# Optimization experiments

Measured on AMD Instinct MI355X. Metric: run time of the kernel, lower is better.

The kernel has to match this reference:

```python
import jax, jax.numpy as jnp
import numpy as np

B, N, NC = 16, 102000, 35        # batch, raw YOLOv7@1280 predictions, num classes
IMG = 1280                        # input image size
CONF_THRESH = 0.25
IOU_THRESH = 0.45
PRE_TOPK = 1024                   # candidates kept before IoU suppression (yolov7 max_nms analogue)
MAX_DET = 300                     # padded detections per image (yolov7 max_det)


def setup_inputs() -> dict:
    key = jax.random.key(0)
    kxy, kwh, kobj, kcls = jax.random.split(key, 4)
    xy = jax.random.uniform(kxy, (B, N, 2), dtype=jnp.float32) * IMG        # box centers in pixels
    wh = jax.random.uniform(kwh, (B, N, 2), dtype=jnp.float32) * 96.0 + 4.0  # box sizes
    obj = jax.random.uniform(kobj, (B, N, 1), dtype=jnp.float32)            # objectness
    cls = jax.random.uniform(kcls, (B, N, NC), dtype=jnp.float32)           # class scores
    pred = jnp.concatenate([xy, wh, obj, cls], axis=-1)  # [B, N, 5+NC]
    return {"pred": pred}


def _xywh2xyxy(xywh):
    xy, wh = xywh[..., :2], xywh[..., 2:4]
    return jnp.concatenate([xy - wh * 0.5, xy + wh * 0.5], axis=-1)


def _iou_matrix(b):
    # b: [K, 4] xyxy -> [K, K] pairwise IoU
    area = jnp.clip(b[:, 2] - b[:, 0], 0.0) * jnp.clip(b[:, 3] - b[:, 1], 0.0)
    lt = jnp.maximum(b[:, None, :2], b[None, :, :2])
    rb = jnp.minimum(b[:, None, 2:], b[None, :, 2:])
    wh = jnp.clip(rb - lt, 0.0)
    inter = wh[..., 0] * wh[..., 1]
    return inter / (area[:, None] + area[None, :] - inter + 1e-7)


def _nms_single(boxes, scores, cls_id):
    # boxes: [N,4] xyxy, scores: [N] (0 where below conf thresh), cls_id: [N] float
    s, idx = jax.lax.top_k(scores, PRE_TOPK)
    b = boxes[idx]
    c = cls_id[idx]
    iou = _iou_matrix(b)              # [K, K]
    valid = s > 0.0
    ar = jnp.arange(PRE_TOPK)

    def body(suppressed, i):
        keep_i = valid[i] & ~suppressed[i]
        suppressed = suppressed | (keep_i & (iou[i] > IOU_THRESH) & (ar > i))
        return suppressed, keep_i

    _, keep = jax.lax.scan(body, jnp.zeros(PRE_TOPK, bool), ar)
    final = jnp.where(keep, s, 0.0)
    fs, fidx = jax.lax.top_k(final, MAX_DET)
    # [MAX_DET, 6] = x1, y1, x2, y2, conf, cls (conf==0 rows are padding)
    return jnp.concatenate([b[fidx], fs[:, None], c[fidx][:, None]], axis=-1)


def reference(pred):
    # yolov7 non_max_suppression, class-agnostic, best-class per box
    boxes = _xywh2xyxy(pred[..., :4])                    # [B, N, 4]
    obj = pred[..., 4]                                   # [B, N]
    cls_scores = pred[..., 5:] * obj[..., None]          # obj_conf * cls_conf
    conf = jnp.max(cls_scores, axis=-1)                  # [B, N]
    cls_id = jnp.argmax(cls_scores, axis=-1).astype(pred.dtype)
    cand = (obj > CONF_THRESH) & (conf > CONF_THRESH)    # candidate filter
    scores = jnp.where(cand, conf, 0.0)
    return jax.vmap(_nms_single)(boxes, scores, cls_id)  # [B, MAX_DET, 6]
```

## Files before the change

### kernel.cpp

```cpp
#include <hip/hip_runtime.h>
#include <stdint.h>

#define BB 16
#define NN 102000
#define NCLS 35
#define RSTRIDE 40
#define PRE 1024
#define CAP 2048
#define MAXDET 300
#define NBUCK 4096
#define CONF_T 0.25f
#define IOU_T 0.45f
#define BUCK_BASE 0x3E800000u
#define SROWS 256
#define HI_BUCK 3584u
#define GL_CAP 16384
#define GCNT_STRIDE 64

#define SCORES_OFF ((size_t)0)
#define SCORES_BYTES ((size_t)BB * NN * 4)
#define GHIST_OFF (SCORES_OFF + SCORES_BYTES)
#define GHIST_BYTES ((size_t)BB * NBUCK * 4)
#define GCNT_OFF (GHIST_OFF + GHIST_BYTES)
#define GCNT_BYTES ((size_t)BB * GCNT_STRIDE * 4)
#define BOXES_OFF (GCNT_OFF + GCNT_BYTES)
#define BOXES_BYTES ((size_t)BB * PRE * 16)
#define SVAL_OFF (BOXES_OFF + BOXES_BYTES)
#define SVAL_BYTES ((size_t)BB * PRE * 4)
#define CLS_OFF (SVAL_OFF + SVAL_BYTES)
#define CLS_BYTES ((size_t)BB * PRE * 4)
#define MASK_OFF (CLS_OFF + CLS_BYTES)
#define MASK_BYTES ((size_t)BB * PRE * 16 * 8)
#define GLIST_OFF (MASK_OFF + MASK_BYTES)
#define GLIST_BYTES ((size_t)BB * GL_CAP * 8)

__device__ __forceinline__ int KS(int i) { return i + (i >> 4); }
#define CAPP (CAP + (CAP >> 4))

__global__ __launch_bounds__(256) void k_score(const float* __restrict__ pred,
                                               float* __restrict__ scores,
                                               unsigned int* __restrict__ ghist,
                                               unsigned int* __restrict__ gcnt,
                                               unsigned long long* __restrict__ glist) {
    __shared__ float4 lds4[SROWS * 9];
    __shared__ unsigned int sWaveCnt[4];
    __shared__ unsigned int sBase;
    int b = blockIdx.y, tid = threadIdx.x;
    int rowBase = blockIdx.x * SROWS;
    int nrows = NN - rowBase; if (nrows > SROWS) nrows = SROWS;
    const float4* gp = (const float4*)(pred + ((size_t)b * NN + rowBase) * RSTRIDE);
    int nf4 = nrows * 9;
    for (int it = tid; it < nf4; it += 256) {
        int r = it / 9;
        int c = it - r * 9;
        lds4[r * 9 + c] = gp[r * 10 + 1 + c];
    }
    __syncthreads();
    float score = 0.0f;
    unsigned int bits = 0u, bk = 0u;
    if (tid < nrows) {
        const float4* row4 = &lds4[tid * 9];
        float4 v0 = row4[0];
        float obj = v0.x;
        if (obj > CONF_T) {
            float best = v0.y * obj;
            best = fmaxf(best, v0.z * obj);
            best = fmaxf(best, v0.w * obj);
#pragma unroll
            for (int c = 1; c < 9; ++c) {
                float4 v = row4[c];
                best = fmaxf(best, v.x * obj);
                best = fmaxf(best, v.y * obj);
                best = fmaxf(best, v.z * obj);
                best = fmaxf(best, v.w * obj);
            }
            if (best > CONF_T) score = best;
        }
        scores[(size_t)b * NN + rowBase + tid] = score;
        if (score > 0.0f) {
            bits = __float_as_uint(score);
            bk = (bits - BUCK_BASE) >> 12;
            if (bk > NBUCK - 1u) bk = NBUCK - 1u;
            atomicAdd(&ghist[b * NBUCK + bk], 1u);
        }
    }
    bool want = (score > 0.0f) && (bk >= HI_BUCK);
    unsigned long long m = __ballot(want);
    int lane = tid & 63, w = tid >> 6;
    if (lane == 0) sWaveCnt[w] = (unsigned int)__popcll(m);
    __syncthreads();
    if (tid == 0) {
        unsigned int tot = sWaveCnt[0] + sWaveCnt[1] + sWaveCnt[2] + sWaveCnt[3];
        sBase = tot ? atomicAdd(&gcnt[b * GCNT_STRIDE], tot) : 0u;
    }
    __syncthreads();
    if (want) {
        unsigned int pos = sBase;
        for (int k = 0; k < w; ++k) pos += sWaveCnt[k];
        pos += (unsigned int)__popcll(m & ((1ull << lane) - 1ull));
        if (pos < GL_CAP)
            glist[(size_t)b * GL_CAP + pos] =
                ((unsigned long long)bits << 32) |
                (unsigned int)(~(unsigned int)(rowBase + tid));
    }
}

__global__ __launch_bounds__(1024) void k_sort(const float* __restrict__ scores,
                                               const unsigned int* __restrict__ ghist,
                                               const unsigned int* __restrict__ gcnt,
                                               const unsigned long long* __restrict__ glist,
                                               const float* __restrict__ pred,
                                               float4* __restrict__ boxesWS,
                                               float* __restrict__ svalWS,
                                               float* __restrict__ clsWS) {
    __shared__ int sA[1024], sB[1024];
    __shared__ int cutSh;
    __shared__ unsigned long long keys[CAPP];
    __shared__ unsigned int nloc;
    int b = blockIdx.x, tid = threadIdx.x;

    const unsigned int* gh = ghist + b * NBUCK;
    int h0 = gh[4 * tid + 0], h1 = gh[4 * tid + 1];
    int h2 = gh[4 * tid + 2], h3 = gh[4 * tid + 3];
    if (tid == 0) { cutSh = 0; nloc = 0u; }
    sA[tid] = h0 + h1 + h2 + h3;
    for (int k = tid; k < CAP; k += 1024) keys[KS(k)] = 0ull;
    __syncthreads();
    int* src = sA;
    int* dst = sB;
    for (int off = 1; off < 1024; off <<= 1) {
        int x = src[tid];
        if (tid + off < 1024) x += src[tid + off];
        dst[tid] = x;
        __syncthreads();
        int* t_ = src; src = dst; dst = t_;
    }
    int nxt = (tid + 1 < 1024) ? src[tid + 1] : 0;
    int s3 = h3 + nxt;
    int s2 = h2 + s3;
    int s1 = h1 + s2;
    int s0 = h0 + s1;
    if (s0 >= PRE && s1 < PRE) cutSh = 4 * tid + 0;
    if (s1 >= PRE && s2 < PRE) cutSh = 4 * tid + 1;
    if (s2 >= PRE && s3 < PRE) cutSh = 4 * tid + 2;
    if (s3 >= PRE && nxt < PRE) cutSh = 4 * tid + 3;
    __syncthreads();
    unsigned int cut = (unsigned int)cutSh;
    unsigned int gn = gcnt[b * GCNT_STRIDE];

    if (cut >= HI_BUCK && gn <= (unsigned int)GL_CAP) {
        int n = (int)gn;
        const unsigned long long* gl = glist + (size_t)b * GL_CAP;
        for (int it = tid; it < n; it += 1024) {
            unsigned long long key = gl[it];
            unsigned int bits = (unsigned int)(key >> 32);
            unsigned int bk = (bits - BUCK_BASE) >> 12;
            if (bk > NBUCK - 1u) bk = NBUCK - 1u;
            if (bk >= cut) {
                unsigned int pos = atomicAdd(&nloc, 1u);
                if (pos < CAP) keys[KS((int)pos)] = key;
            }
        }
    } else {
        const float4* sb4 = (const float4*)(scores + (size_t)b * NN);
        for (int it = tid; it < NN / 4; it += 1024) {
            float4 s4 = sb4[it];
            float sv[4] = {s4.x, s4.y, s4.z, s4.w};
#pragma unroll
            for (int u = 0; u < 4; ++u) {
                float s = sv[u];
                if (s > 0.0f) {
                    unsigned int bits = __float_as_uint(s);
                    unsigned int bk = (bits - BUCK_BASE) >> 12;
                    if (bk > NBUCK - 1u) bk = NBUCK - 1u;
                    if (bk >= cut) {
                        unsigned int pos = atomicAdd(&nloc, 1u);
                        unsigned int idx = (unsigned int)(it * 4 + u);
                        if (pos < CAP)
                            keys[KS((int)pos)] = ((unsigned long long)bits << 32) |
                                                 (unsigned int)(~idx);
                    }
                }
            }
        }
    }
    __syncthreads();

    for (int k = 2; k <= CAP; k <<= 1) {
        for (int j = k >> 1; j > 0; j >>= 1) {
            int p = ((tid & ~(j - 1)) << 1) | (tid & (j - 1));
            int q = p | j;
            int pp = KS(p), qq = KS(q);
            unsigned long long a = keys[pp], c = keys[qq];
            bool desc = (p & k) == 0;
            bool sw = desc ? (a < c) : (a > c);
            if (sw) { keys[pp] = c; keys[qq] = a; }
            __syncthreads();
        }
    }

    unsigned long long key = keys[KS(tid)];
    unsigned int bits = (unsigned int)(key >> 32);
    unsigned int idx = ~(unsigned int)key;
    float sc = __uint_as_float(bits);
    if (bits == 0u || idx >= NN) { idx = 0; sc = 0.0f; }
    const float4* row = (const float4*)(pred + ((size_t)b * NN + idx) * RSTRIDE);
    float4 r0 = row[0];
    float4 r1 = row[1];
    float obj = r1.x;
    float best = r1.y * obj; int bj = 0;
    float p1 = r1.z * obj; if (p1 > best) { best = p1; bj = 1; }
    float p2 = r1.w * obj; if (p2 > best) { best = p2; bj = 2; }
#pragma unroll
    for (int kk = 2; kk <= 9; ++kk) {
        float4 r = row[kk];
        int base = (kk - 2) * 4 + 3;
        float q0 = r.x * obj; if (q0 > best) { best = q0; bj = base + 0; }
        float q1 = r.y * obj; if (q1 > best) { best = q1; bj = base + 1; }
        float q2 = r.z * obj; if (q2 > best) { best = q2; bj = base + 2; }
        float q3 = r.w * obj; if (q3 > best) { best = q3; bj = base + 3; }
    }
    float hx = r0.z * 0.5f;
    float hy = r0.w * 0.5f;
    boxesWS[b * PRE + tid] = make_float4(r0.x - hx, r0.y - hy, r0.x + hx, r0.y + hy);
    svalWS[b * PRE + tid] = sc;
    clsWS[b * PRE + tid] = (float)bj;
}

__global__ __launch_bounds__(256) void k_mask(const float4* __restrict__ boxesWS,
                                              const float* __restrict__ svalWS,
                                              unsigned long long* __restrict__ maskC) {
    __shared__ float bx1[PRE], by1[PRE], bx2[PRE], by2[PRE], bar[PRE], bsv[PRE];
    int b = blockIdx.y, tid = threadIdx.x;
    for (int i = tid; i < PRE; i += 256) {
        float4 bx = boxesWS[b * PRE + i];
        bx1[i] = bx.x; by1[i] = bx.y; bx2[i] = bx.z; by2[i] = bx.w;
        float aw = fmaxf(bx.z - bx.x, 0.0f);
        float ah = fmaxf(bx.w - bx.y, 0.0f);
        bar[i] = aw * ah;
        bsv[i] = svalWS[b * PRE + i];
    }
    __syncthreads();
    int j = blockIdx.x * 4 + (tid >> 6);
    int lane = tid & 63;
    float jx1 = bx1[j], jy1 = by1[j], jx2 = bx2[j], jy2 = by2[j], ja = bar[j];
    unsigned long long* out = maskC + ((size_t)b * PRE + j) * 16;
    for (int c = 0; c < 16; ++c) {
        unsigned long long word = 0ull;
        if (c * 64 < j) {
            int i = c * 64 + lane;
            bool bit = false;
            if (i < j && bsv[i] > 0.0f) {
                float ltx = fmaxf(bx1[i], jx1), lty = fmaxf(by1[i], jy1);
                float rbx = fminf(bx2[i], jx2), rby = fminf(by2[i], jy2);
                float wx = fmaxf(rbx - ltx, 0.0f);
                float wy = fmaxf(rby - lty, 0.0f);
                float inter = wx * wy;
                float denom = ((bar[i] + ja) - inter) + 1e-7f;
                bit = (inter / denom) > IOU_T;
            }
            word = __ballot(bit);
        }
        if (lane == 0) out[c] = word;
    }
}

__global__ __launch_bounds__(1024) void k_nms_out(const float4* __restrict__ boxesWS,
                                                  const float* __restrict__ svalWS,
                                                  const float* __restrict__ clsWS,
                                                  const unsigned long long* __restrict__ maskC,
                                                  float* __restrict__ out) {
    __shared__ unsigned long long supp[16];
    __shared__ int lastch;
    __shared__ int wtot[16], woff[17];
    int b = blockIdx.x, tid = threadIdx.x;
    int lane = tid & 63, w = tid >> 6;
    unsigned long long cm[16];
    const unsigned long long* mrow = maskC + ((size_t)b * PRE + tid) * 16;
#pragma unroll
    for (int k = 0; k < 16; ++k) cm[k] = mrow[k];
    float sv = svalWS[b * PRE + tid];
    if (tid < 16) supp[tid] = 0ull;
    if (tid == 0) lastch = -1;
    __syncthreads();
    for (int it = 0; it < PRE + 2; ++it) {
        bool nb = false;
#pragma unroll
        for (int k = 0; k < 16; ++k) nb |= ((cm[k] & ~supp[k]) != 0ull);
        unsigned long long word = __ballot(nb);
        __syncthreads();
        if (lane == 0) {
            if (word != supp[w]) lastch = it;
            supp[w] = word;
        }
        __syncthreads();
        if (lastch != it) break;
    }
    bool keep = (sv > 0.0f) && !((supp[w] >> lane) & 1ull);
    unsigned long long km = __ballot(keep);
    int lp = __popcll(km & ((lane == 0) ? 0ull : ((1ull << lane) - 1ull)));
    if (lane == 0) wtot[w] = __popcll(km);
    __syncthreads();
    if (tid == 0) {
        int acc = 0;
        for (int k = 0; k < 16; ++k) { woff[k] = acc; acc += wtot[k]; }
        woff[16] = acc;
    }
    __syncthreads();
    int K = woff[16];
    int keptExcl = woff[w] + lp;
    int slot = keep ? keptExcl : (K + (tid - keptExcl));
    if (slot < MAXDET) {
        float4 bx = boxesWS[b * PRE + tid];
        float cv = clsWS[b * PRE + tid];
        float* o = out + ((size_t)b * MAXDET + slot) * 6;
        o[0] = bx.x; o[1] = bx.y; o[2] = bx.z; o[3] = bx.w;
        o[4] = keep ? sv : 0.0f;
        o[5] = cv;
    }
}

extern "C" void kernel_launch(void* const* d_in, const int* in_sizes, int n_in,
                              void* d_out, int out_size, void* d_ws, size_t ws_size,
                              hipStream_t stream) {
    const float* pred = (const float*)d_in[0];
    float* out = (float*)d_out;
    char* ws = (char*)d_ws;
    float* scores = (float*)(ws + SCORES_OFF);
    unsigned int* ghist = (unsigned int*)(ws + GHIST_OFF);
    unsigned int* gcnt = (unsigned int*)(ws + GCNT_OFF);
    float4* boxesWS = (float4*)(ws + BOXES_OFF);
    float* svalWS = (float*)(ws + SVAL_OFF);
    float* clsWS = (float*)(ws + CLS_OFF);
    unsigned long long* maskC = (unsigned long long*)(ws + MASK_OFF);
    unsigned long long* glist = (unsigned long long*)(ws + GLIST_OFF);

    hipMemsetAsync(ws + GHIST_OFF, 0, GHIST_BYTES + GCNT_BYTES, stream);
    k_score<<<dim3((NN + SROWS - 1) / SROWS, BB), 256, 0, stream>>>(pred, scores, ghist,
                                                                   gcnt, glist);
    k_sort<<<BB, 1024, 0, stream>>>(scores, ghist, gcnt, glist, pred,
                                    boxesWS, svalWS, clsWS);
    k_mask<<<dim3(PRE / 4, BB), 256, 0, stream>>>(boxesWS, svalWS, maskC);
    k_nms_out<<<BB, 1024, 0, stream>>>(boxesWS, svalWS, clsWS, maskC, out);
}
```

Measured before the change: 426.7 us.

## Fuse sort, IoU mask and NMS output into one per-image kernel

Merges the sort/gather, IoU mask construction and greedy suppression/output kernels into a single kernel per image, keeping boxes, scores, classes and the suppression mask in registers and LDS instead of global workspace. Each thread now builds its own mask row serially over earlier candidates, replacing the wave-ballot mask kernel. This removes two launches and global round trips but concentrates the quadratic IoU work on only 16 blocks with triangular per-thread imbalance.

```diff
diff --git a/kernel.cpp b/kernel.cpp
--- a/kernel.cpp
+++ b/kernel.cpp
@@ -23,15 +23,7 @@
 #define GHIST_BYTES ((size_t)BB * NBUCK * 4)
 #define GCNT_OFF (GHIST_OFF + GHIST_BYTES)
 #define GCNT_BYTES ((size_t)BB * GCNT_STRIDE * 4)
-#define BOXES_OFF (GCNT_OFF + GCNT_BYTES)
-#define BOXES_BYTES ((size_t)BB * PRE * 16)
-#define SVAL_OFF (BOXES_OFF + BOXES_BYTES)
-#define SVAL_BYTES ((size_t)BB * PRE * 4)
-#define CLS_OFF (SVAL_OFF + SVAL_BYTES)
-#define CLS_BYTES ((size_t)BB * PRE * 4)
-#define MASK_OFF (CLS_OFF + CLS_BYTES)
-#define MASK_BYTES ((size_t)BB * PRE * 16 * 8)
-#define GLIST_OFF (MASK_OFF + MASK_BYTES)
+#define GLIST_OFF (GCNT_OFF + GCNT_BYTES)
 #define GLIST_BYTES ((size_t)BB * GL_CAP * 8)
 
 __device__ __forceinline__ int KS(int i) { return i + (i >> 4); }
@@ -105,19 +97,23 @@
     }
 }
 
-__global__ __launch_bounds__(1024) void k_sort(const float* __restrict__ scores,
-                                               const unsigned int* __restrict__ ghist,
-                                               const unsigned int* __restrict__ gcnt,
-                                               const unsigned long long* __restrict__ glist,
-                                               const float* __restrict__ pred,
-                                               float4* __restrict__ boxesWS,
-                                               float* __restrict__ svalWS,
-                                               float* __restrict__ clsWS) {
+__global__ __launch_bounds__(1024) void k_fused(const float* __restrict__ scores,
+                                                const unsigned int* __restrict__ ghist,
+                                                const unsigned int* __restrict__ gcnt,
+                                                const unsigned long long* __restrict__ glist,
+                                                const float* __restrict__ pred,
+                                                float* __restrict__ out) {
     __shared__ int sA[1024], sB[1024];
+    __shared__ unsigned long long keys[CAPP];
+    __shared__ float bx1[PRE], by1[PRE], bx2[PRE], by2[PRE], bar[PRE], bsv[PRE];
+    __shared__ float scls[PRE];
     __shared__ int cutSh;
-    __shared__ unsigned long long keys[CAPP];
     __shared__ unsigned int nloc;
+    __shared__ unsigned long long supp[16];
+    __shared__ int lastch;
+    __shared__ int wtot[16], woff[17];
     int b = blockIdx.x, tid = threadIdx.x;
+    int lane = tid & 63, w = tid >> 6;
 
     const unsigned int* gh = ghist + b * NBUCK;
     int h0 = gh[4 * tid + 0], h1 = gh[4 * tid + 1];
@@ -200,10 +196,10 @@
     }
 
     unsigned long long key = keys[KS(tid)];
-    unsigned int bits = (unsigned int)(key >> 32);
+    unsigned int kbits = (unsigned int)(key >> 32);
     unsigned int idx = ~(unsigned int)key;
-    float sc = __uint_as_float(bits);
-    if (bits == 0u || idx >= NN) { idx = 0; sc = 0.0f; }
+    float sc = __uint_as_float(kbits);
+    if (kbits == 0u || idx >= NN) { idx = 0; sc = 0.0f; }
     const float4* row = (const float4*)(pred + ((size_t)b * NN + idx) * RSTRIDE);
     float4 r0 = row[0];
     float4 r1 = row[1];
@@ -222,67 +218,40 @@
     }
     float hx = r0.z * 0.5f;
     float hy = r0.w * 0.5f;
-    boxesWS[b * PRE + tid] = make_float4(r0.x - hx, r0.y - hy, r0.x + hx, r0.y + hy);
-    svalWS[b * PRE + tid] = sc;
-    clsWS[b * PRE + tid] = (float)bj;
-}
-
-__global__ __launch_bounds__(256) void k_mask(const float4* __restrict__ boxesWS,
-                                              const float* __restrict__ svalWS,
-                                              unsigned long long* __restrict__ maskC) {
-    __shared__ float bx1[PRE], by1[PRE], bx2[PRE], by2[PRE], bar[PRE], bsv[PRE];
-    int b = blockIdx.y, tid = threadIdx.x;
-    for (int i = tid; i < PRE; i += 256) {
-        float4 bx = boxesWS[b * PRE + i];
-        bx1[i] = bx.x; by1[i] = bx.y; bx2[i] = bx.z; by2[i] = bx.w;
-        float aw = fmaxf(bx.z - bx.x, 0.0f);
-        float ah = fmaxf(bx.w - bx.y, 0.0f);
-        bar[i] = aw * ah;
-        bsv[i] = svalWS[b * PRE + i];
-    }
-    __syncthreads();
-    int j = blockIdx.x * 4 + (tid >> 6);
-    int lane = tid & 63;
-    float jx1 = bx1[j], jy1 = by1[j], jx2 = bx2[j], jy2 = by2[j], ja = bar[j];
-    unsigned long long* out = maskC + ((size_t)b * PRE + j) * 16;
+    float x1 = r0.x - hx, y1 = r0.y - hy, x2 = r0.x + hx, y2 = r0.y + hy;
+    bx1[tid] = x1; by1[tid] = y1; bx2[tid] = x2; by2[tid] = y2;
+    float aw = fmaxf(x2 - x1, 0.0f);
+    float ah = fmaxf(y2 - y1, 0.0f);
+    float ja = aw * ah;
+    bar[tid] = ja;
+    bsv[tid] = sc;
+    scls[tid] = (float)bj;
+    __syncthreads();
+
+    unsigned long long cm[16];
+#pragma unroll
     for (int c = 0; c < 16; ++c) {
         unsigned long long word = 0ull;
-        if (c * 64 < j) {
-            int i = c * 64 + lane;
-            bool bit = false;
-            if (i < j && bsv[i] > 0.0f) {
-                float ltx = fmaxf(bx1[i], jx1), lty = fmaxf(by1[i], jy1);
-                float rbx = fminf(bx2[i], jx2), rby = fminf(by2[i], jy2);
+        int ibase = c * 64;
+        int iend = tid < ibase + 64 ? tid : ibase + 64;
+        for (int i = ibase; i < iend; ++i) {
+            if (bsv[i] > 0.0f) {
+                float ltx = fmaxf(bx1[i], x1), lty = fmaxf(by1[i], y1);
+                float rbx = fminf(bx2[i], x2), rby = fminf(by2[i], y2);
                 float wx = fmaxf(rbx - ltx, 0.0f);
                 float wy = fmaxf(rby - lty, 0.0f);
                 float inter = wx * wy;
                 float denom = ((bar[i] + ja) - inter) + 1e-7f;
-                bit = (inter / denom) > IOU_T;
+                if (inter / denom > IOU_T)
+                    word |= 1ull << (i - ibase);
             }
-            word = __ballot(bit);
-        }
-        if (lane == 0) out[c] = word;
-    }
-}
-
-__global__ __launch_bounds__(1024) void k_nms_out(const float4* __restrict__ boxesWS,
-                                                  const float* __restrict__ svalWS,
-                                                  const float* __restrict__ clsWS,
-                                                  const unsigned long long* __restrict__ maskC,
-                                                  float* __restrict__ out) {
-    __shared__ unsigned long long supp[16];
-    __shared__ int lastch;
-    __shared__ int wtot[16], woff[17];
-    int b = blockIdx.x, tid = threadIdx.x;
-    int lane = tid & 63, w = tid >> 6;
-    unsigned long long cm[16];
-    const unsigned long long* mrow = maskC + ((size_t)b * PRE + tid) * 16;
-#pragma unroll
-    for (int k = 0; k < 16; ++k) cm[k] = mrow[k];
-    float sv = svalWS[b * PRE + tid];
+        }
+        cm[c] = word;
+    }
     if (tid < 16) supp[tid] = 0ull;
     if (tid == 0) lastch = -1;
     __syncthreads();
+
     for (int it = 0; it < PRE + 2; ++it) {
         bool nb = false;
 #pragma unroll
@@ -296,7 +265,7 @@
         __syncthreads();
         if (lastch != it) break;
     }
-    bool keep = (sv > 0.0f) && !((supp[w] >> lane) & 1ull);
+    bool keep = (sc > 0.0f) && !((supp[w] >> lane) & 1ull);
     unsigned long long km = __ballot(keep);
     int lp = __popcll(km & ((lane == 0) ? 0ull : ((1ull << lane) - 1ull)));
     if (lane == 0) wtot[w] = __popcll(km);
@@ -311,12 +280,10 @@
     int keptExcl = woff[w] + lp;
     int slot = keep ? keptExcl : (K + (tid - keptExcl));
     if (slot < MAXDET) {
-        float4 bx = boxesWS[b * PRE + tid];
-        float cv = clsWS[b * PRE + tid];
         float* o = out + ((size_t)b * MAXDET + slot) * 6;
-        o[0] = bx.x; o[1] = bx.y; o[2] = bx.z; o[3] = bx.w;
-        o[4] = keep ? sv : 0.0f;
-        o[5] = cv;
+        o[0] = x1; o[1] = y1; o[2] = x2; o[3] = y2;
+        o[4] = keep ? sc : 0.0f;
+        o[5] = scls[tid];
     }
 }
 
@@ -329,17 +296,10 @@
     float* scores = (float*)(ws + SCORES_OFF);
     unsigned int* ghist = (unsigned int*)(ws + GHIST_OFF);
     unsigned int* gcnt = (unsigned int*)(ws + GCNT_OFF);
-    float4* boxesWS = (float4*)(ws + BOXES_OFF);
-    float* svalWS = (float*)(ws + SVAL_OFF);
-    float* clsWS = (float*)(ws + CLS_OFF);
-    unsigned long long* maskC = (unsigned long long*)(ws + MASK_OFF);
     unsigned long long* glist = (unsigned long long*)(ws + GLIST_OFF);
 
     hipMemsetAsync(ws + GHIST_OFF, 0, GHIST_BYTES + GCNT_BYTES, stream);
     k_score<<<dim3((NN + SROWS - 1) / SROWS, BB), 256, 0, stream>>>(pred, scores, ghist,
                                                                    gcnt, glist);
-    k_sort<<<BB, 1024, 0, stream>>>(scores, ghist, gcnt, glist, pred,
-                                    boxesWS, svalWS, clsWS);
-    k_mask<<<dim3(PRE / 4, BB), 256, 0, stream>>>(boxesWS, svalWS, maskC);
-    k_nms_out<<<BB, 1024, 0, stream>>>(boxesWS, svalWS, clsWS, maskC, out);
+    k_fused<<<BB, 1024, 0, stream>>>(scores, ghist, gcnt, glist, pred, out);
 }
```

Measured after the change: 600.9 us. 1.41x slower.

## Drop global histogram; build high-score histogram in sort kernel, 8-lane-per-row scoring

Applied to the files above, without the earlier changes.

The scoring kernel stops staging rows through LDS and instead assigns 8 lanes per row, each reading one float4 of class scores, with shuffle reductions for the max and wave-local compaction of high-score candidates before a single global atomic per block. The global 4096-bucket histogram and its per-element global atomics are removed, along with the memset of that buffer. The sort kernel now builds a 512-bucket histogram over only the high-score candidate list in LDS, falling back to a full-scores LDS histogram if that list overflows or holds too few entries. This is meant to cut global atomic traffic and the memset, at the cost of a slower fallback path.

```diff
diff --git a/kernel.cpp b/kernel.cpp
--- a/kernel.cpp
+++ b/kernel.cpp
@@ -12,16 +12,14 @@
 #define CONF_T 0.25f
 #define IOU_T 0.45f
 #define BUCK_BASE 0x3E800000u
-#define SROWS 256
 #define HI_BUCK 3584u
+#define HI_BITS 0x3F600000u
 #define GL_CAP 16384
 #define GCNT_STRIDE 64
 
 #define SCORES_OFF ((size_t)0)
 #define SCORES_BYTES ((size_t)BB * NN * 4)
-#define GHIST_OFF (SCORES_OFF + SCORES_BYTES)
-#define GHIST_BYTES ((size_t)BB * NBUCK * 4)
-#define GCNT_OFF (GHIST_OFF + GHIST_BYTES)
+#define GCNT_OFF (SCORES_OFF + SCORES_BYTES)
 #define GCNT_BYTES ((size_t)BB * GCNT_STRIDE * 4)
 #define BOXES_OFF (GCNT_OFF + GCNT_BYTES)
 #define BOXES_BYTES ((size_t)BB * PRE * 16)
@@ -39,74 +37,60 @@
 
 __global__ __launch_bounds__(256) void k_score(const float* __restrict__ pred,
                                                float* __restrict__ scores,
-                                               unsigned int* __restrict__ ghist,
                                                unsigned int* __restrict__ gcnt,
                                                unsigned long long* __restrict__ glist) {
-    __shared__ float4 lds4[SROWS * 9];
-    __shared__ unsigned int sWaveCnt[4];
+    __shared__ unsigned long long wbuf[4 * 64];
+    __shared__ unsigned int wcnt[4], woff[4];
     __shared__ unsigned int sBase;
     int b = blockIdx.y, tid = threadIdx.x;
-    int rowBase = blockIdx.x * SROWS;
-    int nrows = NN - rowBase; if (nrows > SROWS) nrows = SROWS;
-    const float4* gp = (const float4*)(pred + ((size_t)b * NN + rowBase) * RSTRIDE);
-    int nf4 = nrows * 9;
-    for (int it = tid; it < nf4; it += 256) {
-        int r = it / 9;
-        int c = it - r * 9;
-        lds4[r * 9 + c] = gp[r * 10 + 1 + c];
-    }
-    __syncthreads();
-    float score = 0.0f;
-    unsigned int bits = 0u, bk = 0u;
-    if (tid < nrows) {
-        const float4* row4 = &lds4[tid * 9];
-        float4 v0 = row4[0];
-        float obj = v0.x;
-        if (obj > CONF_T) {
-            float best = v0.y * obj;
-            best = fmaxf(best, v0.z * obj);
-            best = fmaxf(best, v0.w * obj);
-#pragma unroll
-            for (int c = 1; c < 9; ++c) {
-                float4 v = row4[c];
-                best = fmaxf(best, v.x * obj);
-                best = fmaxf(best, v.y * obj);
-                best = fmaxf(best, v.z * obj);
-                best = fmaxf(best, v.w * obj);
-            }
-            if (best > CONF_T) score = best;
-        }
-        scores[(size_t)b * NN + rowBase + tid] = score;
-        if (score > 0.0f) {
-            bits = __float_as_uint(score);
-            bk = (bits - BUCK_BASE) >> 12;
-            if (bk > NBUCK - 1u) bk = NBUCK - 1u;
-            atomicAdd(&ghist[b * NBUCK + bk], 1u);
-        }
-    }
-    bool want = (score > 0.0f) && (bk >= HI_BUCK);
-    unsigned long long m = __ballot(want);
     int lane = tid & 63, w = tid >> 6;
-    if (lane == 0) sWaveCnt[w] = (unsigned int)__popcll(m);
+    int sub = lane & 7, rg = lane >> 3;
+    int rowBase = blockIdx.x * 256 + w * 8 + rg;
+    unsigned int wtotal = 0u;
+#pragma unroll
+    for (int p = 0; p < 8; ++p) {
+        int row = rowBase + p * 32;
+        bool rv = row < NN;
+        const float4* rp = (const float4*)(pred + ((size_t)b * NN + row) * RSTRIDE);
+        float4 va = make_float4(0.0f, 0.0f, 0.0f, 0.0f);
+        float4 vb = make_float4(0.0f, 0.0f, 0.0f, 0.0f);
+        if (rv) va = rp[1 + sub];
+        if (rv && sub == 0) vb = rp[9];
+        float f0 = (sub == 0) ? va.y : va.x;
+        float lm = fmaxf(fmaxf(f0, va.y), fmaxf(va.z, va.w));
+        lm = fmaxf(lm, fmaxf(fmaxf(vb.x, vb.y), fmaxf(vb.z, vb.w)));
+        lm = fmaxf(lm, __shfl_xor(lm, 1));
+        lm = fmaxf(lm, __shfl_xor(lm, 2));
+        lm = fmaxf(lm, __shfl_xor(lm, 4));
+        float obj = __shfl(va.x, lane & ~7);
+        float conf = lm * obj;
+        float score = (obj > CONF_T && conf > CONF_T) ? conf : 0.0f;
+        unsigned int bits = __float_as_uint(score);
+        if (sub == 0 && rv) scores[(size_t)b * NN + row] = score;
+        bool want = (sub == 0) && rv && (bits >= HI_BITS) && (score > 0.0f);
+        unsigned long long m = __ballot(want);
+        if (want) {
+            unsigned int off = wtotal + (unsigned int)__popcll(m & ((1ull << lane) - 1ull));
+            wbuf[w * 64 + off] = ((unsigned long long)bits << 32) |
+                                 (unsigned int)(~(unsigned int)row);
+        }
+        wtotal += (unsigned int)__popcll(m);
+    }
+    if (lane == 0) wcnt[w] = wtotal;
     __syncthreads();
     if (tid == 0) {
-        unsigned int tot = sWaveCnt[0] + sWaveCnt[1] + sWaveCnt[2] + sWaveCnt[3];
-        sBase = tot ? atomicAdd(&gcnt[b * GCNT_STRIDE], tot) : 0u;
-    }
-    __syncthreads();
-    if (want) {
-        unsigned int pos = sBase;
-        for (int k = 0; k < w; ++k) pos += sWaveCnt[k];
-        pos += (unsigned int)__popcll(m & ((1ull << lane) - 1ull));
-        if (pos < GL_CAP)
-            glist[(size_t)b * GL_CAP + pos] =
-                ((unsigned long long)bits << 32) |
-                (unsigned int)(~(unsigned int)(rowBase + tid));
+        unsigned int acc = 0;
+        for (int k = 0; k < 4; ++k) { woff[k] = acc; acc += wcnt[k]; }
+        sBase = acc ? atomicAdd(&gcnt[b * GCNT_STRIDE], acc) : 0u;
+    }
+    __syncthreads();
+    for (unsigned int i = (unsigned int)lane; i < wtotal; i += 64u) {
+        unsigned int pos = sBase + woff[w] + i;
+        if (pos < GL_CAP) glist[(size_t)b * GL_CAP + pos] = wbuf[w * 64 + i];
     }
 }
 
 __global__ __launch_bounds__(1024) void k_sort(const float* __restrict__ scores,
-                                               const unsigned int* __restrict__ ghist,
                                                const unsigned int* __restrict__ gcnt,
                                                const unsigned long long* __restrict__ glist,
                                                const float* __restrict__ pred,
@@ -114,55 +98,97 @@
                                                float* __restrict__ svalWS,
                                                float* __restrict__ clsWS) {
     __shared__ int sA[1024], sB[1024];
+    __shared__ unsigned int hh[512];
+    __shared__ unsigned int fh[NBUCK];
     __shared__ int cutSh;
     __shared__ unsigned long long keys[CAPP];
     __shared__ unsigned int nloc;
     int b = blockIdx.x, tid = threadIdx.x;
-
-    const unsigned int* gh = ghist + b * NBUCK;
-    int h0 = gh[4 * tid + 0], h1 = gh[4 * tid + 1];
-    int h2 = gh[4 * tid + 2], h3 = gh[4 * tid + 3];
-    if (tid == 0) { cutSh = 0; nloc = 0u; }
-    sA[tid] = h0 + h1 + h2 + h3;
+    unsigned int gn = gcnt[b * GCNT_STRIDE];
+    if (tid == 0) { cutSh = -1; nloc = 0u; }
+    if (tid < 512) hh[tid] = 0u;
     for (int k = tid; k < CAP; k += 1024) keys[KS(k)] = 0ull;
     __syncthreads();
-    int* src = sA;
-    int* dst = sB;
-    for (int off = 1; off < 1024; off <<= 1) {
-        int x = src[tid];
-        if (tid + off < 1024) x += src[tid + off];
-        dst[tid] = x;
-        __syncthreads();
-        int* t_ = src; src = dst; dst = t_;
-    }
-    int nxt = (tid + 1 < 1024) ? src[tid + 1] : 0;
-    int s3 = h3 + nxt;
-    int s2 = h2 + s3;
-    int s1 = h1 + s2;
-    int s0 = h0 + s1;
-    if (s0 >= PRE && s1 < PRE) cutSh = 4 * tid + 0;
-    if (s1 >= PRE && s2 < PRE) cutSh = 4 * tid + 1;
-    if (s2 >= PRE && s3 < PRE) cutSh = 4 * tid + 2;
-    if (s3 >= PRE && nxt < PRE) cutSh = 4 * tid + 3;
-    __syncthreads();
-    unsigned int cut = (unsigned int)cutSh;
-    unsigned int gn = gcnt[b * GCNT_STRIDE];
-
-    if (cut >= HI_BUCK && gn <= (unsigned int)GL_CAP) {
-        int n = (int)gn;
-        const unsigned long long* gl = glist + (size_t)b * GL_CAP;
-        for (int it = tid; it < n; it += 1024) {
+    const unsigned long long* gl = glist + (size_t)b * GL_CAP;
+    bool fast = (gn <= (unsigned int)GL_CAP);
+    if (fast) {
+        for (unsigned int it = tid; it < gn; it += 1024u) {
+            unsigned int bits = (unsigned int)(gl[it] >> 32);
+            unsigned int bk = (bits - BUCK_BASE) >> 12;
+            if (bk > NBUCK - 1u) bk = NBUCK - 1u;
+            atomicAdd(&hh[bk - HI_BUCK], 1u);
+        }
+        __syncthreads();
+        if (tid < 512) sA[tid] = (int)hh[tid];
+        __syncthreads();
+        int* src = sA; int* dst = sB;
+        for (int off = 1; off < 512; off <<= 1) {
+            if (tid < 512) {
+                int x = src[tid];
+                if (tid + off < 512) x += src[tid + off];
+                dst[tid] = x;
+            }
+            __syncthreads();
+            int* t_ = src; src = dst; dst = t_;
+        }
+        if (tid < 512) {
+            int suf = src[tid];
+            int nx = (tid + 1 < 512) ? src[tid + 1] : 0;
+            if (suf >= PRE && nx < PRE) cutSh = (int)HI_BUCK + tid;
+        }
+        __syncthreads();
+    }
+    int cut = cutSh;
+    if (fast && cut >= (int)HI_BUCK) {
+        for (unsigned int it = tid; it < gn; it += 1024u) {
             unsigned long long key = gl[it];
             unsigned int bits = (unsigned int)(key >> 32);
             unsigned int bk = (bits - BUCK_BASE) >> 12;
             if (bk > NBUCK - 1u) bk = NBUCK - 1u;
-            if (bk >= cut) {
+            if ((int)bk >= cut) {
                 unsigned int pos = atomicAdd(&nloc, 1u);
                 if (pos < CAP) keys[KS((int)pos)] = key;
             }
         }
     } else {
-        const float4* sb4 = (const float4*)(scores + (size_t)b * NN);
+        for (int k = tid; k < NBUCK; k += 1024) fh[k] = 0u;
+        __syncthreads();
+        const float* sb = scores + (size_t)b * NN;
+        for (int it = tid; it < NN; it += 1024) {
+            float s = sb[it];
+            if (s > 0.0f) {
+                unsigned int bits = __float_as_uint(s);
+                unsigned int bk = (bits - BUCK_BASE) >> 12;
+                if (bk > NBUCK - 1u) bk = NBUCK - 1u;
+                atomicAdd(&fh[bk], 1u);
+            }
+        }
+        __syncthreads();
+        int h0 = fh[4 * tid + 0], h1 = fh[4 * tid + 1];
+        int h2 = fh[4 * tid + 2], h3 = fh[4 * tid + 3];
+        if (tid == 0) cutSh = 0;
+        sA[tid] = h0 + h1 + h2 + h3;
+        __syncthreads();
+        int* src = sA; int* dst = sB;
+        for (int off = 1; off < 1024; off <<= 1) {
+            int x = src[tid];
+            if (tid + off < 1024) x += src[tid + off];
+            dst[tid] = x;
+            __syncthreads();
+            int* t_ = src; src = dst; dst = t_;
+        }
+        int nxt = (tid + 1 < 1024) ? src[tid + 1] : 0;
+        int s3 = h3 + nxt;
+        int s2 = h2 + s3;
+        int s1 = h1 + s2;
+        int s0 = h0 + s1;
+        if (s0 >= PRE && s1 < PRE) cutSh = 4 * tid + 0;
+        if (s1 >= PRE && s2 < PRE) cutSh = 4 * tid + 1;
+        if (s2 >= PRE && s3 < PRE) cutSh = 4 * tid + 2;
+        if (s3 >= PRE && nxt < PRE) cutSh = 4 * tid + 3;
+        __syncthreads();
+        unsigned int ccut = (unsigned int)cutSh;
+        const float4* sb4 = (const float4*)sb;
         for (int it = tid; it < NN / 4; it += 1024) {
             float4 s4 = sb4[it];
             float sv[4] = {s4.x, s4.y, s4.z, s4.w};
@@ -173,7 +199,7 @@
                     unsigned int bits = __float_as_uint(s);
                     unsigned int bk = (bits - BUCK_BASE) >> 12;
                     if (bk > NBUCK - 1u) bk = NBUCK - 1u;
-                    if (bk >= cut) {
+                    if (bk >= ccut) {
                         unsigned int pos = atomicAdd(&nloc, 1u);
                         unsigned int idx = (unsigned int)(it * 4 + u);
                         if (pos < CAP)
@@ -327,7 +353,6 @@
     float* out = (float*)d_out;
     char* ws = (char*)d_ws;
     float* scores = (float*)(ws + SCORES_OFF);
-    unsigned int* ghist = (unsigned int*)(ws + GHIST_OFF);
     unsigned int* gcnt = (unsigned int*)(ws + GCNT_OFF);
     float4* boxesWS = (float4*)(ws + BOXES_OFF);
     float* svalWS = (float*)(ws + SVAL_OFF);
@@ -335,10 +360,9 @@
     unsigned long long* maskC = (unsigned long long*)(ws + MASK_OFF);
     unsigned long long* glist = (unsigned long long*)(ws + GLIST_OFF);
 
-    hipMemsetAsync(ws + GHIST_OFF, 0, GHIST_BYTES + GCNT_BYTES, stream);
-    k_score<<<dim3((NN + SROWS - 1) / SROWS, BB), 256, 0, stream>>>(pred, scores, ghist,
-                                                                   gcnt, glist);
-    k_sort<<<BB, 1024, 0, stream>>>(scores, ghist, gcnt, glist, pred,
+    hipMemsetAsync(ws + GCNT_OFF, 0, GCNT_BYTES, stream);
+    k_score<<<dim3((NN + 255) / 256, BB), 256, 0, stream>>>(pred, scores, gcnt, glist);
+    k_sort<<<BB, 1024, 0, stream>>>(scores, gcnt, glist, pred,
                                     boxesWS, svalWS, clsWS);
     k_mask<<<dim3(PRE / 4, BB), 256, 0, stream>>>(boxesWS, svalWS, maskC);
     k_nms_out<<<BB, 1024, 0, stream>>>(boxesWS, svalWS, clsWS, maskC, out);
```

New measurement: 418.5 us. Within noise of the previous version (-1.9%).
